# Kernel optimization log

Measured on AMD Instinct MI355X. Metric: run time of the kernel, lower is better.

## Reference

```python
import jax, jax.numpy as jnp
import numpy as np

N_NODES = 200000
N_EDGES = 3200000
IN_CH, HID, HID2, OUT = 12, 64, 32, 2


def setup_inputs() -> dict:
    key = jax.random.key(0)
    ks = jax.random.split(key, 10)
    x = jax.random.normal(ks[0], (N_NODES, IN_CH), dtype=jnp.float32)
    edge_index = jax.random.randint(ks[1], (2, N_EDGES), 0, N_NODES, dtype=jnp.int64)
    s = lambda k, shp, fan_in: jax.random.normal(k, shp, jnp.float32) / np.sqrt(fan_in)
    return {
        "x": x,
        "edge_index": edge_index,
        # SAGEConv1: lin_l (neighbor, with bias) and lin_r (root, no bias)
        "w1l": s(ks[2], (IN_CH, HID), IN_CH),
        "b1": jnp.zeros((HID,), jnp.float32),
        "w1r": s(ks[3], (IN_CH, HID), IN_CH),
        # SAGEConv2
        "w2l": s(ks[4], (HID, HID2), HID),
        "b2": jnp.zeros((HID2,), jnp.float32),
        "w2r": s(ks[5], (HID, HID2), HID),
        # classifier
        "wc": s(ks[6], (HID2, OUT), HID2),
        "bc": jnp.zeros((OUT,), jnp.float32),
    }


def _sage_conv(x, src, dst, wl, bl, wr):
    """PyG SAGEConv with mean aggregation: lin_l(mean_{j in N(i)} x_j) + lin_r(x_i)."""
    n = x.shape[0]
    # gather source features and scatter-sum to destinations: [E, F] -> [N, F]
    agg = jax.ops.segment_sum(x[src], dst, num_segments=n)
    deg = jax.ops.segment_sum(jnp.ones((src.shape[0],), x.dtype), dst, num_segments=n)
    mean = agg / jnp.maximum(deg, 1.0)[:, None]
    return mean @ wl + bl + x @ wr


def reference(x, edge_index, w1l, b1, w1r, w2l, b2, w2r, wc, bc):
    src, dst = edge_index[0], edge_index[1]
    h = jax.nn.relu(_sage_conv(x, src, dst, w1l, b1, w1r))   # [N, 64]
    h = jax.nn.relu(_sage_conv(h, src, dst, w2l, b2, w2r))   # [N, 32]
    return h @ wc + bc                                        # [N, 2]
```

## Files before the change

### kernel.cpp

```cpp
#include <hip/hip_runtime.h>
#include <hip/hip_bf16.h>


#define IN_CH 12
#define HID   64
#define HID2  32

using f32x4  = __attribute__((ext_vector_type(4))) float;
using bf16x8 = __attribute__((ext_vector_type(8))) short;

__device__ __forceinline__ unsigned short f2bf(float f) {
  union { float f; unsigned int u; } cv; cv.f = f;
  unsigned int b = cv.u;
  return (unsigned short)((b + 0x7fffu + ((b >> 16) & 1u)) >> 16);
}
__device__ __forceinline__ unsigned int packbf(float a, float b) {
  return (unsigned int)f2bf(a) | ((unsigned int)f2bf(b) << 16);
}

__global__ void detect_i64(const int* __restrict__ ei, int* __restrict__ flag) {
  if ((blockIdx.x | threadIdx.x) == 0) {
    *flag = ((ei[1] | ei[3] | ei[5] | ei[7]) == 0) ? 1 : 0;
  }
}

__global__ __launch_bounds__(256) void p1_hist(
    const int* __restrict__ ei, int* __restrict__ bcnt,
    const int* __restrict__ flag, int E, int nb) {
  __shared__ int lh[256];
  int t = threadIdx.x;
  lh[t] = 0;
  __syncthreads();
  int f64 = *flag;
  size_t base = (size_t)blockIdx.x * 8192;
  for (int i = 0; i < 32; ++i) {
    size_t e = base + (size_t)i * 256 + t;
    if (e < (size_t)E) {
      int dst = f64 ? ei[2 * ((size_t)E + e)] : ei[(size_t)E + e];
      atomicAdd(&lh[dst >> 10], 1);
    }
  }
  __syncthreads();
  if (t < nb && lh[t]) atomicAdd(&bcnt[t], lh[t]);
}

__global__ __launch_bounds__(256) void scan_buckets(
    const int* __restrict__ bcnt, int* __restrict__ bstart,
    int* __restrict__ bcur, int nb) {
  __shared__ int s[256];
  int t = threadIdx.x;
  int v = (t < nb) ? bcnt[t] : 0;
  s[t] = v;
  __syncthreads();
  for (int d = 1; d < 256; d <<= 1) {
    int a = (t >= d) ? s[t - d] : 0;
    __syncthreads();
    s[t] += a;
    __syncthreads();
  }
  int excl = s[t] - v;
  if (t < nb) { bstart[t] = excl; bcur[t] = excl; }
  if (t == 255) bstart[nb] = s[255];
}

__global__ __launch_bounds__(256) void p2_bin(
    const int* __restrict__ ei, int* __restrict__ bcur,
    unsigned int* __restrict__ binned, const int* __restrict__ flag,
    int E, int nb) {
  __shared__ int lh[256];
  __shared__ int lbase[256];
  int t = threadIdx.x;
  lh[t] = 0;
  __syncthreads();
  int f64 = *flag;
  size_t base = (size_t)blockIdx.x * 8192;
  for (int i = 0; i < 32; ++i) {
    size_t e = base + (size_t)i * 256 + t;
    if (e < (size_t)E) {
      int dst = f64 ? ei[2 * ((size_t)E + e)] : ei[(size_t)E + e];
      atomicAdd(&lh[dst >> 10], 1);
    }
  }
  __syncthreads();
  if (t < nb) {
    int c = lh[t];
    lbase[t] = c ? atomicAdd(&bcur[t], c) : 0;
  }
  __syncthreads();
  lh[t] = 0;
  __syncthreads();
  for (int i = 0; i < 32; ++i) {
    size_t e = base + (size_t)i * 256 + t;
    if (e < (size_t)E) {
      int src, dst;
      if (f64) { src = ei[2 * e]; dst = ei[2 * ((size_t)E + e)]; }
      else     { src = ei[e];     dst = ei[(size_t)E + e]; }
      int b = dst >> 10;
      int lp = atomicAdd(&lh[b], 1);
      binned[lbase[b] + lp] = ((unsigned int)(dst & 1023) << 18) | (unsigned int)src;
    }
  }
}

__global__ __launch_bounds__(1024) void p3_build(
    const unsigned int* __restrict__ binned, const int* __restrict__ bstart,
    int* __restrict__ deg, int* __restrict__ off, int* __restrict__ csr, int N) {
  __shared__ int cnt[1024];
  __shared__ int s[1024];
  __shared__ int cur[1024];
  int t = threadIdx.x;
  int b = blockIdx.x;
  int nbase = b << 10;
  int estart = bstart[b], eend = bstart[b + 1];
  cnt[t] = 0;
  __syncthreads();
  for (int e = estart + t; e < eend; e += 1024) {
    unsigned int p = binned[e];
    atomicAdd(&cnt[p >> 18], 1);
  }
  __syncthreads();
  int v = cnt[t];
  s[t] = v;
  __syncthreads();
  for (int d = 1; d < 1024; d <<= 1) {
    int a = (t >= d) ? s[t - d] : 0;
    __syncthreads();
    s[t] += a;
    __syncthreads();
  }
  int excl = s[t] - v;
  int node = nbase + t;
  if (node < N) { deg[node] = v; off[node] = estart + excl; }
  cur[t] = estart + excl;
  __syncthreads();
  for (int e = estart + t; e < eend; e += 1024) {
    unsigned int p = binned[e];
    int pos = atomicAdd(&cur[p >> 18], 1);
    csr[pos] = (int)(p & 0x3FFFFu);
  }
}

__global__ __launch_bounds__(256) void xcast(
    const float* __restrict__ x, unsigned int* __restrict__ inb32, int N) {
  int i = blockIdx.x * 256 + threadIdx.x;
  if (i >= N * 8) return;
  int n = i >> 3, cp = i & 7;
  unsigned int w = 0;
  if (cp < 6) {
    float2 v = *(const float2*)(x + (size_t)n * IN_CH + cp * 2);
    w = packbf(v.x, v.y);
  }
  inb32[(size_t)n * 16 + 8 + cp] = w;
}

__global__ __launch_bounds__(256) void agg1_mean(
    const int* __restrict__ off, const int* __restrict__ deg,
    const int* __restrict__ csr, unsigned int* __restrict__ inb32, int N) {
  int tid = blockIdx.x * 256 + threadIdx.x;
  int node = tid >> 3;
  int l = tid & 7;
  if (node >= N) return;
  unsigned int* row = inb32 + (size_t)node * 16;
  if (l >= 6) { row[l] = 0; return; }
  int start = off[node], d = deg[node];
  const unsigned int* xg = inb32 + 8 + l;
  float a0 = 0.f, a1 = 0.f;
  for (int j = 0; j < d; j += 8) {
    unsigned int w[8];
#pragma unroll
    for (int k = 0; k < 8; ++k) {
      int jj = j + k;
      int s = csr[start + (jj < d ? jj : 0)];
      unsigned int wv = xg[(size_t)s * 16];
      w[k] = (jj < d) ? wv : 0u;
    }
#pragma unroll
    for (int k = 0; k < 8; ++k) {
      a0 += __uint_as_float(w[k] << 16);
      a1 += __uint_as_float(w[k] & 0xffff0000u);
    }
  }
  float inv = 1.0f / fmaxf((float)d, 1.0f);
  row[l] = packbf(a0 * inv, a1 * inv);
}

__global__ void prep_frags(
    const float* __restrict__ w1l, const float* __restrict__ w1r,
    const float* __restrict__ w2l, const float* __restrict__ w2r,
    unsigned int* __restrict__ wfrag) {
  int f = blockIdx.x, l = threadIdx.x;
  int q = l >> 4, c = l & 15;
  unsigned int out[4];
#pragma unroll
  for (int p = 0; p < 4; ++p) {
    float v[2];
#pragma unroll
    for (int s = 0; s < 2; ++s) {
      int i = 2 * p + s;
      float val = 0.f;
      if (f < 4) {
        int k = q * 8 + i, ch = f * 16 + c;
        if (k < 12) val = w1l[k * HID + ch];
        else if (k >= 16 && k < 28) val = w1r[(k - 16) * HID + ch];
      } else {
        int t2 = (f - 4) >> 1, half = (f - 4) & 1;
        int k = half * 32 + q * 8 + i;
        int oc = t2 * 16 + c;
        val = (t2 < 2) ? w2l[k * HID2 + oc] : w2r[k * HID2 + (oc - 32)];
      }
      v[s] = val;
    }
    out[p] = packbf(v[0], v[1]);
  }
  *(uint4*)&wfrag[(f * 64 + l) * 4] = make_uint4(out[0], out[1], out[2], out[3]);
}

__global__ __launch_bounds__(256) void layer1_mfma(
    const unsigned short* __restrict__ in_bf, const unsigned int* __restrict__ wfrag,
    const float* __restrict__ b1, const float* __restrict__ b2,
    unsigned short* __restrict__ g, unsigned short* __restrict__ r, int N) {
  __shared__ unsigned int s_h[4][512];
  int t = threadIdx.x, wave = t >> 6, l = t & 63;
  int q = l >> 4, c = l & 15;
  int swz = c & 7;

  union FU { uint4 u4; bf16x8 v; } fu;
  bf16x8 a1[4], a2[8];
#pragma unroll
  for (int f = 0; f < 4; ++f) { fu.u4 = ((const uint4*)wfrag)[f * 64 + l]; a1[f] = fu.v; }
#pragma unroll
  for (int f = 0; f < 8; ++f) { fu.u4 = ((const uint4*)wfrag)[(4 + f) * 64 + l]; a2[f] = fu.v; }

  f32x4 c1[4], c2[4];
#pragma unroll
  for (int t1 = 0; t1 < 4; ++t1) {
    float4 bv = *(const float4*)(b1 + t1 * 16 + q * 4);
    c1[t1][0] = bv.x; c1[t1][1] = bv.y; c1[t1][2] = bv.z; c1[t1][3] = bv.w;
  }
#pragma unroll
  for (int t2 = 0; t2 < 4; ++t2) {
    if (t2 < 2) { c2[t2][0] = 0.f; c2[t2][1] = 0.f; c2[t2][2] = 0.f; c2[t2][3] = 0.f; }
    else {
      float4 bv = *(const float4*)(b2 + (t2 - 2) * 16 + q * 4);
      c2[t2][0] = bv.x; c2[t2][1] = bv.y; c2[t2][2] = bv.z; c2[t2][3] = bv.w;
    }
  }

  int ntiles = (N + 15) >> 4;
  for (int tile = blockIdx.x * 4 + wave; tile < ntiles; tile += gridDim.x * 4) {
    int node_g = tile * 16 + c;
    int ng = node_g < N ? node_g : N - 1;
    fu.u4 = ((const uint4*)in_bf)[(size_t)ng * 4 + q];
    bf16x8 bfrag = fu.v;

#pragma unroll
    for (int t1 = 0; t1 < 4; ++t1) {
      f32x4 d = __builtin_amdgcn_mfma_f32_16x16x32_bf16(a1[t1], bfrag, c1[t1], 0, 0, 0);
      unsigned int lo = packbf(fmaxf(d[0], 0.f), fmaxf(d[1], 0.f));
      unsigned int hi = packbf(fmaxf(d[2], 0.f), fmaxf(d[3], 0.f));
      int gr = (t1 * 2 + (q >> 1)) ^ swz;
      int idx = c * 32 + gr * 4 + (q & 1) * 2;
      *(uint2*)&s_h[wave][idx] = make_uint2(lo, hi);
    }
    __builtin_amdgcn_wave_barrier();

    bf16x8 hf0, hf1;
    fu.u4 = *(const uint4*)&s_h[wave][c * 32 + ((q) ^ swz) * 4];       hf0 = fu.v;
    fu.u4 = *(const uint4*)&s_h[wave][c * 32 + ((4 + q) ^ swz) * 4];   hf1 = fu.v;

    if (node_g < N) {
      size_t gb = (size_t)node_g * HID2;
#pragma unroll
      for (int t2 = 0; t2 < 4; ++t2) {
        f32x4 d = __builtin_amdgcn_mfma_f32_16x16x32_bf16(a2[t2 * 2 + 0], hf0, c2[t2], 0, 0, 0);
        d = __builtin_amdgcn_mfma_f32_16x16x32_bf16(a2[t2 * 2 + 1], hf1, d, 0, 0, 0);
        unsigned int lo = packbf(d[0], d[1]);
        unsigned int hi = packbf(d[2], d[3]);
        unsigned short* dst = (t2 < 2) ? g : r;
        int ch = (t2 & 1) * 16 + q * 4;
        *(uint2*)(dst + gb + ch) = make_uint2(lo, hi);
      }
    }
    __builtin_amdgcn_wave_barrier();
  }
}

__global__ __launch_bounds__(256) void agg2_final(
    const int* __restrict__ off, const int* __restrict__ deg,
    const int* __restrict__ csr, const unsigned short* __restrict__ g,
    const unsigned short* __restrict__ r, const float* __restrict__ wc,
    const float* __restrict__ bc, float* __restrict__ out, int N) {
  int tid = blockIdx.x * 256 + threadIdx.x;
  int node = tid >> 5;
  int lane = tid & 31;
  if (node >= N) return;
  int start = off[node], d = deg[node];
  const unsigned short* gl = g + lane;
  float acc = 0.f;
  for (int j = 0; j < d; j += 8) {
    unsigned int w[8];
#pragma unroll
    for (int k = 0; k < 8; ++k) {
      int jj = j + k;
      int s = csr[start + (jj < d ? jj : 0)];
      unsigned int wv = (unsigned int)gl[(size_t)s * HID2];
      w[k] = (jj < d) ? wv : 0u;
    }
#pragma unroll
    for (int k = 0; k < 8; ++k) acc += __uint_as_float(w[k] << 16);
  }
  float dg = fmaxf((float)d, 1.0f);
  unsigned int rw = r[(size_t)node * HID2 + lane];
  float v = fmaxf(acc / dg + __uint_as_float(rw << 16), 0.0f);
  float p0 = v * wc[lane * 2 + 0];
  float p1 = v * wc[lane * 2 + 1];
#pragma unroll
  for (int o2 = 16; o2 > 0; o2 >>= 1) {
    p0 += __shfl_down(p0, o2, 32);
    p1 += __shfl_down(p1, o2, 32);
  }
  if (lane == 0) {
    out[(size_t)node * 2 + 0] = p0 + bc[0];
    out[(size_t)node * 2 + 1] = p1 + bc[1];
  }
}

extern "C" void kernel_launch(void* const* d_in, const int* in_sizes, int n_in,
                              void* d_out, int out_size, void* d_ws, size_t ws_size,
                              hipStream_t stream) {
  const float* x   = (const float*)d_in[0];
  const int*   ei  = (const int*)d_in[1];
  const float* w1l = (const float*)d_in[2];
  const float* b1  = (const float*)d_in[3];
  const float* w1r = (const float*)d_in[4];
  const float* w2l = (const float*)d_in[5];
  const float* b2  = (const float*)d_in[6];
  const float* w2r = (const float*)d_in[7];
  const float* wc  = (const float*)d_in[8];
  const float* bc  = (const float*)d_in[9];
  float* out = (float*)d_out;

  int N = in_sizes[0] / IN_CH;
  int E = in_sizes[1] / 2;
  int nb = (N + 1023) >> 10;

  int* deg    = (int*)d_ws;
  int* off    = deg + N;
  int* bmeta  = off + N;
  int* bcnt   = bmeta;
  int* bstart = bmeta + 256;
  int* bcur   = bmeta + 513;
  int* flag   = bmeta + 769;
  int* csr    = bmeta + 772;
  unsigned int* binned = (unsigned int*)(csr + E);
  unsigned int* inb32  = binned + E;
  unsigned short* inb  = (unsigned short*)inb32;
  unsigned short* g    = (unsigned short*)(inb32 + (size_t)N * 16);
  unsigned short* r    = g + (size_t)N * HID2;
  unsigned int* wfrag  = (unsigned int*)(r + (size_t)N * HID2);

  hipMemsetAsync(bcnt, 0, 256 * sizeof(int), stream);
  detect_i64<<<1, 64, 0, stream>>>(ei, flag);

  xcast<<<((size_t)N * 8 + 255) / 256, 256, 0, stream>>>(x, inb32, N);
  prep_frags<<<12, 64, 0, stream>>>(w1l, w1r, w2l, w2r, wfrag);

  int ebblocks = (E + 8191) / 8192;
  p1_hist<<<ebblocks, 256, 0, stream>>>(ei, bcnt, flag, E, nb);
  scan_buckets<<<1, 256, 0, stream>>>(bcnt, bstart, bcur, nb);
  p2_bin<<<ebblocks, 256, 0, stream>>>(ei, bcur, binned, flag, E, nb);
  p3_build<<<nb, 1024, 0, stream>>>(binned, bstart, deg, off, csr, N);

  agg1_mean<<<((size_t)N * 8 + 255) / 256, 256, 0, stream>>>(off, deg, csr, inb32, N);

  layer1_mfma<<<1024, 256, 0, stream>>>(inb, wfrag, b1, b2, g, r, N);

  agg2_final<<<((size_t)N * 32 + 255) / 256, 256, 0, stream>>>(
      off, deg, csr, g, r, wc, bc, out, N);
}
```

Before: 342.3 us.

## Fuse preprocessing kernels and widen per-thread gathers in aggregation kernels

Merges the int64 detection, histogram, x-to-bf16 cast and weight-fragment prep into one launch. Each p1/p2 block now checks the index width inline instead of reading a flag. Both aggregation kernels switch to 8-byte (uint2) gathers: agg1 uses 4 lanes per node instead of 8, and agg2 uses 8 lanes instead of 32, with the classifier dot product done in registers. The goal is fewer launches and fewer, wider memory transactions per neighbor, at the cost of less thread-level parallelism per node.

```diff
diff --git a/kernel.cpp b/kernel.cpp
--- a/kernel.cpp
+++ b/kernel.cpp
@@ -17,31 +17,73 @@
 __device__ __forceinline__ unsigned int packbf(float a, float b) {
   return (unsigned int)f2bf(a) | ((unsigned int)f2bf(b) << 16);
 }
-
-__global__ void detect_i64(const int* __restrict__ ei, int* __restrict__ flag) {
-  if ((blockIdx.x | threadIdx.x) == 0) {
-    *flag = ((ei[1] | ei[3] | ei[5] | ei[7]) == 0) ? 1 : 0;
-  }
-}
-
-__global__ __launch_bounds__(256) void p1_hist(
+__device__ __forceinline__ int detect_f64(const int* __restrict__ ei) {
+  return ((ei[1] | ei[3] | ei[5] | ei[7]) == 0) ? 1 : 0;
+}
+
+__global__ __launch_bounds__(256) void fused_pre(
     const int* __restrict__ ei, int* __restrict__ bcnt,
-    const int* __restrict__ flag, int E, int nb) {
-  __shared__ int lh[256];
+    const float* __restrict__ x, unsigned int* __restrict__ inb32,
+    const float* __restrict__ w1l, const float* __restrict__ w1r,
+    const float* __restrict__ w2l, const float* __restrict__ w2r,
+    unsigned int* __restrict__ wfrag, int E, int N, int nb,
+    int histB, int xcastB) {
+  int bid = blockIdx.x;
   int t = threadIdx.x;
-  lh[t] = 0;
-  __syncthreads();
-  int f64 = *flag;
-  size_t base = (size_t)blockIdx.x * 8192;
-  for (int i = 0; i < 32; ++i) {
-    size_t e = base + (size_t)i * 256 + t;
-    if (e < (size_t)E) {
-      int dst = f64 ? ei[2 * ((size_t)E + e)] : ei[(size_t)E + e];
-      atomicAdd(&lh[dst >> 10], 1);
-    }
-  }
-  __syncthreads();
-  if (t < nb && lh[t]) atomicAdd(&bcnt[t], lh[t]);
+  if (bid < histB) {
+    __shared__ int lh[256];
+    lh[t] = 0;
+    __syncthreads();
+    int f64 = detect_f64(ei);
+    size_t base = (size_t)bid * 8192;
+    for (int i = 0; i < 32; ++i) {
+      size_t e = base + (size_t)i * 256 + t;
+      if (e < (size_t)E) {
+        int dst = f64 ? ei[2 * ((size_t)E + e)] : ei[(size_t)E + e];
+        atomicAdd(&lh[dst >> 10], 1);
+      }
+    }
+    __syncthreads();
+    if (t < nb && lh[t]) atomicAdd(&bcnt[t], lh[t]);
+  } else if (bid < histB + xcastB) {
+    int i = (bid - histB) * 256 + t;
+    if (i < N * 8) {
+      int n = i >> 3, cp = i & 7;
+      unsigned int w = 0;
+      if (cp < 6) {
+        float2 v = *(const float2*)(x + (size_t)n * IN_CH + cp * 2);
+        w = packbf(v.x, v.y);
+      }
+      inb32[(size_t)n * 16 + 8 + cp] = w;
+    }
+  } else {
+    if (t >= 64) return;
+    int f = bid - histB - xcastB;
+    int q = t >> 4, c = t & 15;
+    unsigned int out[4];
+#pragma unroll
+    for (int p = 0; p < 4; ++p) {
+      float v[2];
+#pragma unroll
+      for (int s = 0; s < 2; ++s) {
+        int i = 2 * p + s;
+        float val = 0.f;
+        if (f < 4) {
+          int k = q * 8 + i, ch = f * 16 + c;
+          if (k < 12) val = w1l[k * HID + ch];
+          else if (k >= 16 && k < 28) val = w1r[(k - 16) * HID + ch];
+        } else {
+          int t2 = (f - 4) >> 1, half = (f - 4) & 1;
+          int k = half * 32 + q * 8 + i;
+          int oc = t2 * 16 + c;
+          val = (t2 < 2) ? w2l[k * HID2 + oc] : w2r[k * HID2 + (oc - 32)];
+        }
+        v[s] = val;
+      }
+      out[p] = packbf(v[0], v[1]);
+    }
+    *(uint4*)&wfrag[(f * 64 + t) * 4] = make_uint4(out[0], out[1], out[2], out[3]);
+  }
 }
 
 __global__ __launch_bounds__(256) void scan_buckets(
@@ -65,14 +107,13 @@
 
 __global__ __launch_bounds__(256) void p2_bin(
     const int* __restrict__ ei, int* __restrict__ bcur,
-    unsigned int* __restrict__ binned, const int* __restrict__ flag,
-    int E, int nb) {
+    unsigned int* __restrict__ binned, int E, int nb) {
   __shared__ int lh[256];
   __shared__ int lbase[256];
   int t = threadIdx.x;
   lh[t] = 0;
   __syncthreads();
-  int f64 = *flag;
+  int f64 = detect_f64(ei);
   size_t base = (size_t)blockIdx.x * 8192;
   for (int i = 0; i < 32; ++i) {
     size_t e = base + (size_t)i * 256 + t;
@@ -140,79 +181,41 @@
   }
 }
 
-__global__ __launch_bounds__(256) void xcast(
-    const float* __restrict__ x, unsigned int* __restrict__ inb32, int N) {
-  int i = blockIdx.x * 256 + threadIdx.x;
-  if (i >= N * 8) return;
-  int n = i >> 3, cp = i & 7;
-  unsigned int w = 0;
-  if (cp < 6) {
-    float2 v = *(const float2*)(x + (size_t)n * IN_CH + cp * 2);
-    w = packbf(v.x, v.y);
-  }
-  inb32[(size_t)n * 16 + 8 + cp] = w;
-}
-
 __global__ __launch_bounds__(256) void agg1_mean(
     const int* __restrict__ off, const int* __restrict__ deg,
     const int* __restrict__ csr, unsigned int* __restrict__ inb32, int N) {
   int tid = blockIdx.x * 256 + threadIdx.x;
-  int node = tid >> 3;
-  int l = tid & 7;
+  int node = tid >> 2;
+  int l = tid & 3;
   if (node >= N) return;
   unsigned int* row = inb32 + (size_t)node * 16;
-  if (l >= 6) { row[l] = 0; return; }
+  if (l == 3) { row[6] = 0; row[7] = 0; return; }
   int start = off[node], d = deg[node];
-  const unsigned int* xg = inb32 + 8 + l;
-  float a0 = 0.f, a1 = 0.f;
-  for (int j = 0; j < d; j += 8) {
-    unsigned int w[8];
-#pragma unroll
-    for (int k = 0; k < 8; ++k) {
-      int jj = j + k;
-      int s = csr[start + (jj < d ? jj : 0)];
-      unsigned int wv = xg[(size_t)s * 16];
-      w[k] = (jj < d) ? wv : 0u;
-    }
-#pragma unroll
-    for (int k = 0; k < 8; ++k) {
-      a0 += __uint_as_float(w[k] << 16);
-      a1 += __uint_as_float(w[k] & 0xffff0000u);
+  float a0 = 0.f, a1 = 0.f, a2 = 0.f, a3 = 0.f;
+  if (d > 0) {
+    const uint2* xg = (const uint2*)(inb32 + 8) + l;
+    for (int j = 0; j < d; j += 8) {
+      uint2 w[8];
+#pragma unroll
+      for (int k = 0; k < 8; ++k) {
+        int jj = j + k;
+        int s = csr[start + (jj < d ? jj : 0)];
+        uint2 wv = xg[(size_t)s * 8];
+        w[k].x = (jj < d) ? wv.x : 0u;
+        w[k].y = (jj < d) ? wv.y : 0u;
+      }
+#pragma unroll
+      for (int k = 0; k < 8; ++k) {
+        a0 += __uint_as_float(w[k].x << 16);
+        a1 += __uint_as_float(w[k].x & 0xffff0000u);
+        a2 += __uint_as_float(w[k].y << 16);
+        a3 += __uint_as_float(w[k].y & 0xffff0000u);
+      }
     }
   }
   float inv = 1.0f / fmaxf((float)d, 1.0f);
-  row[l] = packbf(a0 * inv, a1 * inv);
-}
-
-__global__ void prep_frags(
-    const float* __restrict__ w1l, const float* __restrict__ w1r,
-    const float* __restrict__ w2l, const float* __restrict__ w2r,
-    unsigned int* __restrict__ wfrag) {
-  int f = blockIdx.x, l = threadIdx.x;
-  int q = l >> 4, c = l & 15;
-  unsigned int out[4];
-#pragma unroll
-  for (int p = 0; p < 4; ++p) {
-    float v[2];
-#pragma unroll
-    for (int s = 0; s < 2; ++s) {
-      int i = 2 * p + s;
-      float val = 0.f;
-      if (f < 4) {
-        int k = q * 8 + i, ch = f * 16 + c;
-        if (k < 12) val = w1l[k * HID + ch];
-        else if (k >= 16 && k < 28) val = w1r[(k - 16) * HID + ch];
-      } else {
-        int t2 = (f - 4) >> 1, half = (f - 4) & 1;
-        int k = half * 32 + q * 8 + i;
-        int oc = t2 * 16 + c;
-        val = (t2 < 2) ? w2l[k * HID2 + oc] : w2r[k * HID2 + (oc - 32)];
-      }
-      v[s] = val;
-    }
-    out[p] = packbf(v[0], v[1]);
-  }
-  *(uint4*)&wfrag[(f * 64 + l) * 4] = make_uint4(out[0], out[1], out[2], out[3]);
+  *(uint2*)(row + 2 * l) =
+      make_uint2(packbf(a0 * inv, a1 * inv), packbf(a2 * inv, a3 * inv));
 }
 
 __global__ __launch_bounds__(256) void layer1_mfma(
@@ -287,37 +290,52 @@
 
 __global__ __launch_bounds__(256) void agg2_final(
     const int* __restrict__ off, const int* __restrict__ deg,
-    const int* __restrict__ csr, const unsigned short* __restrict__ g,
-    const unsigned short* __restrict__ r, const float* __restrict__ wc,
+    const int* __restrict__ csr, const unsigned int* __restrict__ g32,
+    const unsigned int* __restrict__ r32, const float* __restrict__ wc,
     const float* __restrict__ bc, float* __restrict__ out, int N) {
   int tid = blockIdx.x * 256 + threadIdx.x;
-  int node = tid >> 5;
-  int lane = tid & 31;
+  int node = tid >> 3;
+  int lane = tid & 7;
   if (node >= N) return;
   int start = off[node], d = deg[node];
-  const unsigned short* gl = g + lane;
-  float acc = 0.f;
-  for (int j = 0; j < d; j += 8) {
-    unsigned int w[8];
-#pragma unroll
-    for (int k = 0; k < 8; ++k) {
-      int jj = j + k;
-      int s = csr[start + (jj < d ? jj : 0)];
-      unsigned int wv = (unsigned int)gl[(size_t)s * HID2];
-      w[k] = (jj < d) ? wv : 0u;
-    }
-#pragma unroll
-    for (int k = 0; k < 8; ++k) acc += __uint_as_float(w[k] << 16);
+  float a0 = 0.f, a1 = 0.f, a2 = 0.f, a3 = 0.f;
+  if (d > 0) {
+    const uint2* gl = (const uint2*)g32 + lane;
+    for (int j = 0; j < d; j += 8) {
+      uint2 w[8];
+#pragma unroll
+      for (int k = 0; k < 8; ++k) {
+        int jj = j + k;
+        int s = csr[start + (jj < d ? jj : 0)];
+        uint2 wv = gl[(size_t)s * 8];
+        w[k].x = (jj < d) ? wv.x : 0u;
+        w[k].y = (jj < d) ? wv.y : 0u;
+      }
+#pragma unroll
+      for (int k = 0; k < 8; ++k) {
+        a0 += __uint_as_float(w[k].x << 16);
+        a1 += __uint_as_float(w[k].x & 0xffff0000u);
+        a2 += __uint_as_float(w[k].y << 16);
+        a3 += __uint_as_float(w[k].y & 0xffff0000u);
+      }
+    }
   }
   float dg = fmaxf((float)d, 1.0f);
-  unsigned int rw = r[(size_t)node * HID2 + lane];
-  float v = fmaxf(acc / dg + __uint_as_float(rw << 16), 0.0f);
-  float p0 = v * wc[lane * 2 + 0];
-  float p1 = v * wc[lane * 2 + 1];
-#pragma unroll
-  for (int o2 = 16; o2 > 0; o2 >>= 1) {
-    p0 += __shfl_down(p0, o2, 32);
-    p1 += __shfl_down(p1, o2, 32);
+  float inv = 1.0f / dg;
+  uint2 rw = *((const uint2*)r32 + (size_t)node * 8 + lane);
+  float v0 = fmaxf(a0 * inv + __uint_as_float(rw.x << 16), 0.0f);
+  float v1 = fmaxf(a1 * inv + __uint_as_float(rw.x & 0xffff0000u), 0.0f);
+  float v2 = fmaxf(a2 * inv + __uint_as_float(rw.y << 16), 0.0f);
+  float v3 = fmaxf(a3 * inv + __uint_as_float(rw.y & 0xffff0000u), 0.0f);
+  int ch = lane * 4;
+  float p0 = v0 * wc[(ch + 0) * 2] + v1 * wc[(ch + 1) * 2] +
+             v2 * wc[(ch + 2) * 2] + v3 * wc[(ch + 3) * 2];
+  float p1 = v0 * wc[(ch + 0) * 2 + 1] + v1 * wc[(ch + 1) * 2 + 1] +
+             v2 * wc[(ch + 2) * 2 + 1] + v3 * wc[(ch + 3) * 2 + 1];
+#pragma unroll
+  for (int o2 = 4; o2 > 0; o2 >>= 1) {
+    p0 += __shfl_down(p0, o2, 8);
+    p1 += __shfl_down(p1, o2, 8);
   }
   if (lane == 0) {
     out[(size_t)node * 2 + 0] = p0 + bc[0];
@@ -350,31 +368,31 @@
   int* bcnt   = bmeta;
   int* bstart = bmeta + 256;
   int* bcur   = bmeta + 513;
-  int* flag   = bmeta + 769;
   int* csr    = bmeta + 772;
   unsigned int* binned = (unsigned int*)(csr + E);
   unsigned int* inb32  = binned + E;
   unsigned short* inb  = (unsigned short*)inb32;
-  unsigned short* g    = (unsigned short*)(inb32 + (size_t)N * 16);
-  unsigned short* r    = g + (size_t)N * HID2;
-  unsigned int* wfrag  = (unsigned int*)(r + (size_t)N * HID2);
+  unsigned int* g32    = inb32 + (size_t)N * 16;
+  unsigned short* g    = (unsigned short*)g32;
+  unsigned int* r32    = g32 + (size_t)N * 16;
+  unsigned short* r    = (unsigned short*)r32;
+  unsigned int* wfrag  = r32 + (size_t)N * 16;
 
   hipMemsetAsync(bcnt, 0, 256 * sizeof(int), stream);
-  detect_i64<<<1, 64, 0, stream>>>(ei, flag);
-
-  xcast<<<((size_t)N * 8 + 255) / 256, 256, 0, stream>>>(x, inb32, N);
-  prep_frags<<<12, 64, 0, stream>>>(w1l, w1r, w2l, w2r, wfrag);
-
-  int ebblocks = (E + 8191) / 8192;
-  p1_hist<<<ebblocks, 256, 0, stream>>>(ei, bcnt, flag, E, nb);
+
+  int histB  = (E + 8191) / 8192;
+  int xcastB = (N * 8 + 255) / 256;
+  fused_pre<<<histB + xcastB + 12, 256, 0, stream>>>(
+      ei, bcnt, x, inb32, w1l, w1r, w2l, w2r, wfrag, E, N, nb, histB, xcastB);
+
   scan_buckets<<<1, 256, 0, stream>>>(bcnt, bstart, bcur, nb);
-  p2_bin<<<ebblocks, 256, 0, stream>>>(ei, bcur, binned, flag, E, nb);
+  p2_bin<<<histB, 256, 0, stream>>>(ei, bcur, binned, E, nb);
   p3_build<<<nb, 1024, 0, stream>>>(binned, bstart, deg, off, csr, N);
 
-  agg1_mean<<<((size_t)N * 8 + 255) / 256, 256, 0, stream>>>(off, deg, csr, inb32, N);
+  agg1_mean<<<((size_t)N * 4 + 255) / 256, 256, 0, stream>>>(off, deg, csr, inb32, N);
 
   layer1_mfma<<<1024, 256, 0, stream>>>(inb, wfrag, b1, b2, g, r, N);
 
-  agg2_final<<<((size_t)N * 32 + 255) / 256, 256, 0, stream>>>(
-      off, deg, csr, g, r, wc, bc, out, N);
-}
+  agg2_final<<<((size_t)N * 8 + 255) / 256, 256, 0, stream>>>(
+      off, deg, csr, g32, r32, wc, bc, out, N);
+}
```

After: 328.6 us. 1.04x faster.
